# Kernel optimization log

Measured on AMD Instinct MI355X. Metric: run time of the kernel, lower is better.

Reference implementation:

```python
import jax, jax.numpy as jnp
import numpy as np

B, T, D = 4, 2048, 1024
H = 16
HD = D // H  # 64

def setup_inputs() -> dict:
    key = jax.random.key(0)
    k1, k2, k3, k4, k5 = jax.random.split(key, 5)
    s = 1.0 / np.sqrt(D)
    return {
        "x": jax.random.normal(k1, (B, T, D), dtype=jnp.float32),
        "Wqkv": jax.random.normal(k2, (D, 3 * D), dtype=jnp.float32) * s,
        "bqkv": jnp.zeros((3 * D,), dtype=jnp.float32),
        "Wproj": jax.random.normal(k3, (D, D), dtype=jnp.float32) * s,
        "bproj": jnp.zeros((D,), dtype=jnp.float32),
    }

def reference(x, Wqkv, bqkv, Wproj, bproj):
    Bq, Tq, C = x.shape
    qkv = x @ Wqkv + bqkv                       # [B,T,3D]
    qkv = qkv.reshape(Bq, Tq, 3, H, HD).transpose(2, 0, 3, 1, 4)  # [3,B,H,T,hd]
    q, k, v = qkv[0], qkv[1], qkv[2]
    scale = 1.0 / np.sqrt(HD)
    att = jnp.einsum("bhqd,bhkd->bhqk", q, k) * scale  # [B,H,T,T]
    causal = jnp.tril(jnp.ones((Tq, Tq), dtype=bool))
    att = jnp.where(causal[None, None], att, -jnp.inf)
    att = jax.nn.softmax(att, axis=-1)
    out = jnp.einsum("bhqk,bhkd->bhqd", att, v)        # [B,H,T,hd]
    out = out.transpose(0, 2, 1, 3).reshape(Bq, Tq, C)
    return out @ Wproj + bproj
```

## Files before the change

### kernel.cpp

```cpp
#include <hip/hip_runtime.h>

typedef float f32x4 __attribute__((ext_vector_type(4)));
typedef __bf16 bf16x8 __attribute__((ext_vector_type(8)));
typedef __bf16 bf16x4 __attribute__((ext_vector_type(4)));

#define B_ 4
#define T_ 2048
#define D_ 1024
#define H_ 16
#define HD_ 64

__device__ __forceinline__ void gload_lds16(const void* g, void* l) {
  __builtin_amdgcn_global_load_lds(
      (const __attribute__((address_space(1))) void*)g,
      (__attribute__((address_space(3))) void*)l, 16, 0, 0);
}

__global__ __launch_bounds__(256) void k_cvt_f32_bf16(
    const float* __restrict__ in, __bf16* __restrict__ out, int n4) {
  int i = blockIdx.x * blockDim.x + threadIdx.x;
  int stride = gridDim.x * blockDim.x;
  for (; i < n4; i += stride) {
    float4 v = reinterpret_cast<const float4*>(in)[i];
    bf16x4 o = { (__bf16)v.x, (__bf16)v.y, (__bf16)v.z, (__bf16)v.w };
    reinterpret_cast<bf16x4*>(out)[i] = o;
  }
}

template <typename Tin>
__global__ __launch_bounds__(256) void k_transpose_bf16(
    const Tin* __restrict__ in, __bf16* __restrict__ out,
    int R, int C, long inb, long outb) {
  __shared__ alignas(16) __bf16 lds[64 * 68];
  const int t = threadIdx.x;
  in  += (long)blockIdx.z * inb;
  out += (long)blockIdx.z * outb;
  const int r0 = blockIdx.y * 64, c0 = blockIdx.x * 64;
#pragma unroll
  for (int i = 0; i < 16; ++i) {
    int e = i * 256 + t, row = e >> 6, col = e & 63;
    lds[row * 68 + col] = (__bf16)(float)in[(long)(r0 + row) * C + c0 + col];
  }
  __syncthreads();
#pragma unroll
  for (int i = 0; i < 16; ++i) {
    int e = i * 256 + t, orow = e >> 6, ocol = e & 63;
    out[(long)(c0 + orow) * R + r0 + ocol] = lds[ocol * 68 + orow];
  }
}

template <int EPI>
__global__ __launch_bounds__(256) void k_gemm_bt(
    const __bf16* __restrict__ A, const __bf16* __restrict__ Bt,
    const float* __restrict__ bias, void* __restrict__ Cout,
    __bf16* __restrict__ vout, int M, int N, int K) {
  __shared__ alignas(16) __bf16 As[2][128 * 32];
  __shared__ alignas(16) __bf16 Bs[2][128 * 32];
  const int t = threadIdx.x;
  const int w = t >> 6, l = t & 63;
  const int g = l >> 4, r16 = l & 15;
  const int wr = w >> 1, wc = w & 1;
  const int m0 = blockIdx.y * 128, n0 = blockIdx.x * 128;

  f32x4 acc[4][4];
#pragma unroll
  for (int i = 0; i < 4; ++i)
#pragma unroll
    for (int j = 0; j < 4; ++j) acc[i][j] = (f32x4){0.f, 0.f, 0.f, 0.f};

  const int arow = t >> 2;
  const int acol = ((t & 3) ^ ((t >> 3) & 3)) * 8;
  const char* Ag = (const char*)(A + (long)(m0 + arow) * K + acol);
  const char* Bg = (const char*)(Bt + (long)(n0 + arow) * K + acol);
  const long rowskip = (long)64 * K * 2;
  const int rdsw = (g ^ ((r16 >> 1) & 3)) * 8;

  auto stage = [&](int buf, long koff) {
    char* AsW = (char*)As[buf] + w * 1024;
    char* BsW = (char*)Bs[buf] + w * 1024;
    gload_lds16(Ag + koff, AsW);
    gload_lds16(Ag + koff + rowskip, AsW + 4096);
    gload_lds16(Bg + koff, BsW);
    gload_lds16(Bg + koff + rowskip, BsW + 4096);
  };

  stage(0, 0);
  __syncthreads();

  for (int kt = 0; kt < K; kt += 32) {
    const int cur = (kt >> 5) & 1;
    if (kt + 32 < K) stage(cur ^ 1, (long)(kt + 32) * 2);
    bf16x8 af[4], bfr[4];
#pragma unroll
    for (int mi = 0; mi < 4; ++mi)
      af[mi] = *reinterpret_cast<const bf16x8*>(
          &As[cur][(wr * 64 + mi * 16 + r16) * 32 + rdsw]);
#pragma unroll
    for (int ni = 0; ni < 4; ++ni)
      bfr[ni] = *reinterpret_cast<const bf16x8*>(
          &Bs[cur][(wc * 64 + ni * 16 + r16) * 32 + rdsw]);
    __builtin_amdgcn_s_setprio(1);
#pragma unroll
    for (int mi = 0; mi < 4; ++mi)
#pragma unroll
      for (int ni = 0; ni < 4; ++ni)
        acc[mi][ni] = __builtin_amdgcn_mfma_f32_16x16x32_bf16(af[mi], bfr[ni], acc[mi][ni], 0, 0, 0);
    __builtin_amdgcn_s_setprio(0);
    __syncthreads();
  }

  if (EPI == 0) {
    const int which = n0 >> 10;
    __bf16* qkvb = (__bf16*)Cout;
#pragma unroll
    for (int mi = 0; mi < 4; ++mi) {
#pragma unroll
      for (int ni = 0; ni < 4; ++ni) {
        const int n = n0 + wc * 64 + ni * 16 + r16;
        const float bv = bias[n];
        f32x4 c = acc[mi][ni];
        const int rem = n & 1023, h = rem >> 6, hd = rem & 63;
        const int mbase = m0 + wr * 64 + mi * 16 + g * 4;
        const int b = mbase >> 11, tt0 = mbase & 2047;
        if (which < 2) {
#pragma unroll
          for (int r = 0; r < 4; ++r)
            qkvb[((long)((which * B_ + b) * H_ + h) * T_ + tt0 + r) * HD_ + hd] =
                (__bf16)(c[r] + bv);
        } else {
          bf16x4 pk = { (__bf16)(c[0] + bv), (__bf16)(c[1] + bv),
                        (__bf16)(c[2] + bv), (__bf16)(c[3] + bv) };
          *reinterpret_cast<bf16x4*>(
              &vout[(((long)b * H_ + h) * HD_ + hd) * T_ + tt0]) = pk;
        }
      }
    }
  } else {
    float* O = (float*)Cout;
#pragma unroll
    for (int mi = 0; mi < 4; ++mi) {
#pragma unroll
      for (int ni = 0; ni < 4; ++ni) {
        const int n = n0 + wc * 64 + ni * 16 + r16;
        const float bv = bias[n];
        f32x4 c = acc[mi][ni];
        const int mbase = m0 + wr * 64 + mi * 16 + g * 4;
#pragma unroll
        for (int r = 0; r < 4; ++r) O[(long)(mbase + r) * N + n] = c[r] + bv;
      }
    }
  }
}

__device__ __forceinline__ void soft_side(
    const f32x4 (&s)[4], float& lrun, char* pw, bool diag, int qrel,
    int g, int r16, bf16x8& pa0, bf16x8& pa1) {
  float p[4][4];
#pragma unroll
  for (int nf = 0; nf < 4; ++nf) {
#pragma unroll
    for (int rr = 0; rr < 4; ++rr) {
      float x = s[nf][rr];
      if (diag) x = (nf * 16 + 4 * g + rr <= qrel + r16) ? x : -1e30f;
      p[nf][rr] = exp2f(x);
    }
  }
  const float ps0 = (p[0][0] + p[0][1]) + (p[0][2] + p[0][3]);
  const float ps1 = (p[1][0] + p[1][1]) + (p[1][2] + p[1][3]);
  const float ps2 = (p[2][0] + p[2][1]) + (p[2][2] + p[2][3]);
  const float ps3 = (p[3][0] + p[3][1]) + (p[3][2] + p[3][3]);
  lrun += (ps0 + ps1) + (ps2 + ps3);

#pragma unroll
  for (int nf = 0; nf < 4; ++nf) {
    bf16x4 pk = { (__bf16)p[nf][0], (__bf16)p[nf][1],
                  (__bf16)p[nf][2], (__bf16)p[nf][3] };
    const int slot = 2 * nf + (g >> 1);
    *reinterpret_cast<bf16x4*>(
        pw + r16 * 128 + ((slot ^ (r16 & 7)) << 4) + (g & 1) * 8) = pk;
  }
  pa0 = *reinterpret_cast<const bf16x8*>(pw + r16 * 128 + ((g ^ (r16 & 7)) << 4));
  pa1 = *reinterpret_cast<const bf16x8*>(pw + r16 * 128 + (((4 + g) ^ (r16 & 7)) << 4));
}

__global__ __launch_bounds__(256) void k_attn(
    const __bf16* __restrict__ q, const __bf16* __restrict__ k,
    const __bf16* __restrict__ vt, __bf16* __restrict__ o) {
  __shared__ alignas(16) __bf16 Ks[2][64 * 64];
  __shared__ alignas(16) __bf16 Vs[2][64 * 64];
  __shared__ alignas(16) __bf16 Ps[4][16 * 64];
  const int t = threadIdx.x, w = t >> 6, l = t & 63;
  const int g = l >> 4, r16 = l & 15;
  const int bh = blockIdx.x, pr = blockIdx.y;
  const int qtA = 31 - pr, qtB = pr;
  const int qbaseA = qtA * 64 + w * 16;
  const int qbaseB = qtB * 64 + w * 16;
  const float sc = 0.125f * 1.44269504088896341f;

  auto scale8 = [&](bf16x8 v) {
    bf16x8 r;
#pragma unroll
    for (int j = 0; j < 8; ++j) r[j] = (__bf16)((float)v[j] * sc);
    return r;
  };
  const __bf16* qpA = q + ((long)bh * T_ + qbaseA + r16) * HD_ + g * 8;
  const bf16x8 aqA0 = scale8(*reinterpret_cast<const bf16x8*>(qpA));
  const bf16x8 aqA1 = scale8(*reinterpret_cast<const bf16x8*>(qpA + 32));
  const __bf16* qpB = q + ((long)bh * T_ + qbaseB + r16) * HD_ + g * 8;
  const bf16x8 aqB0 = scale8(*reinterpret_cast<const bf16x8*>(qpB));
  const bf16x8 aqB1 = scale8(*reinterpret_cast<const bf16x8*>(qpB + 32));

  f32x4 oA[4], oB[4];
  float lA = 0.f, lB = 0.f;
#pragma unroll
  for (int i = 0; i < 4; ++i) {
    oA[i] = (f32x4){0.f, 0.f, 0.f, 0.f};
    oB[i] = (f32x4){0.f, 0.f, 0.f, 0.f};
  }

  const int srow = t >> 3, sslot = t & 7;
  const int sswz = sslot ^ (srow & 7);
  const char* kg = (const char*)(k + ((long)bh * T_ + srow) * HD_) + sswz * 16;
  const char* vg = (const char*)(vt + ((long)bh * HD_ + srow) * T_) + sswz * 16;
  char* pw = (char*)&Ps[w][0];

  auto stage = [&](int buf, int kv0) {
    char* Kd = (char*)Ks[buf] + w * 1024;
    char* Vd = (char*)Vs[buf] + w * 1024;
    gload_lds16(kg + (long)kv0 * 128, Kd);
    gload_lds16(kg + (long)kv0 * 128 + 32 * 128, Kd + 4096);
    gload_lds16(vg + (long)kv0 * 2, Vd);
    gload_lds16(vg + (long)kv0 * 2 + 32 * (long)T_ * 2, Vd + 4096);
  };

  stage(0, 0);
  __syncthreads();

  const int ntile = qtA + 1;
  for (int it = 0; it < ntile; ++it) {
    const int cur = it & 1;
    if (it + 1 < ntile) stage(cur ^ 1, (it + 1) * 64);
    const char* Kc = (const char*)Ks[cur];
    const char* Vc = (const char*)Vs[cur];
    const bool doB = (it <= qtB);

    f32x4 sA[4], sB[4];
    __builtin_amdgcn_s_setprio(1);
#pragma unroll
    for (int nf = 0; nf < 4; ++nf) {
      const char* kb = Kc + (nf * 16 + r16) * 128;
      const bf16x8 b0 = *reinterpret_cast<const bf16x8*>(kb + ((g ^ (r16 & 7)) << 4));
      const bf16x8 b1 = *reinterpret_cast<const bf16x8*>(kb + (((4 + g) ^ (r16 & 7)) << 4));
      f32x4 z = (f32x4){0.f, 0.f, 0.f, 0.f};
      z = __builtin_amdgcn_mfma_f32_16x16x32_bf16(b0, aqA0, z, 0, 0, 0);
      z = __builtin_amdgcn_mfma_f32_16x16x32_bf16(b1, aqA1, z, 0, 0, 0);
      sA[nf] = z;
      if (doB) {
        f32x4 zb = (f32x4){0.f, 0.f, 0.f, 0.f};
        zb = __builtin_amdgcn_mfma_f32_16x16x32_bf16(b0, aqB0, zb, 0, 0, 0);
        zb = __builtin_amdgcn_mfma_f32_16x16x32_bf16(b1, aqB1, zb, 0, 0, 0);
        sB[nf] = zb;
      }
    }
    __builtin_amdgcn_s_setprio(0);

    bf16x8 paA0, paA1, paB0, paB1;
    soft_side(sA, lA, pw, it == qtA, qbaseA - it * 64, g, r16, paA0, paA1);
    if (doB)
      soft_side(sB, lB, pw, it == qtB, qbaseB - it * 64, g, r16, paB0, paB1);

    __builtin_amdgcn_s_setprio(1);
#pragma unroll
    for (int nf = 0; nf < 4; ++nf) {
      const char* vb = Vc + (nf * 16 + r16) * 128;
      const bf16x8 v0 = *reinterpret_cast<const bf16x8*>(vb + ((g ^ (r16 & 7)) << 4));
      const bf16x8 v1 = *reinterpret_cast<const bf16x8*>(vb + (((4 + g) ^ (r16 & 7)) << 4));
      oA[nf] = __builtin_amdgcn_mfma_f32_16x16x32_bf16(paA0, v0, oA[nf], 0, 0, 0);
      oA[nf] = __builtin_amdgcn_mfma_f32_16x16x32_bf16(paA1, v1, oA[nf], 0, 0, 0);
      if (doB) {
        oB[nf] = __builtin_amdgcn_mfma_f32_16x16x32_bf16(paB0, v0, oB[nf], 0, 0, 0);
        oB[nf] = __builtin_amdgcn_mfma_f32_16x16x32_bf16(paB1, v1, oB[nf], 0, 0, 0);
      }
    }
    __builtin_amdgcn_s_setprio(0);
    __syncthreads();
  }

  lA += __shfl_xor(lA, 16, 64);
  lA += __shfl_xor(lA, 32, 64);
  lB += __shfl_xor(lB, 16, 64);
  lB += __shfl_xor(lB, 32, 64);
  const float invA = 1.f / lA, invB = 1.f / lB;
  float invAq[4], invBq[4];
#pragma unroll
  for (int rr = 0; rr < 4; ++rr) {
    invAq[rr] = __shfl(invA, 4 * g + rr, 64);
    invBq[rr] = __shfl(invB, 4 * g + rr, 64);
  }
  const int b = bh >> 4, h = bh & 15;
#pragma unroll
  for (int nf = 0; nf < 4; ++nf) {
    const int hd = nf * 16 + r16;
#pragma unroll
    for (int rr = 0; rr < 4; ++rr) {
      const int ttA = qbaseA + g * 4 + rr;
      o[((long)b * T_ + ttA) * D_ + h * HD_ + hd] = (__bf16)(oA[nf][rr] * invAq[rr]);
      const int ttB = qbaseB + g * 4 + rr;
      o[((long)b * T_ + ttB) * D_ + h * HD_ + hd] = (__bf16)(oB[nf][rr] * invBq[rr]);
    }
  }
}

extern "C" void kernel_launch(void* const* d_in, const int* in_sizes, int n_in,
                              void* d_out, int out_size, void* d_ws, size_t ws_size,
                              hipStream_t stream) {
  (void)in_sizes; (void)n_in; (void)out_size; (void)ws_size;
  const float* x     = (const float*)d_in[0];
  const float* Wqkv  = (const float*)d_in[1];
  const float* bqkv  = (const float*)d_in[2];
  const float* Wproj = (const float*)d_in[3];
  const float* bproj = (const float*)d_in[4];
  float* out = (float*)d_out;

  const long MT = (long)B_ * T_;
  __bf16* xb     = (__bf16*)d_ws;
  __bf16* wqkvt  = xb + MT * D_;
  __bf16* wprojt = wqkvt + (long)3 * D_ * D_;
  __bf16* qkvb   = wprojt + (long)D_ * D_;
  __bf16* vtb    = qkvb + (long)2 * B_ * H_ * T_ * HD_;
  __bf16* attno  = vtb + (long)B_ * H_ * HD_ * T_;

  k_cvt_f32_bf16<<<2048, 256, 0, stream>>>(x, xb, (int)(MT * D_ / 4));
  k_transpose_bf16<float><<<dim3(48, 16, 1), 256, 0, stream>>>(Wqkv, wqkvt, D_, 3 * D_, 0, 0);
  k_transpose_bf16<float><<<dim3(16, 16, 1), 256, 0, stream>>>(Wproj, wprojt, D_, D_, 0, 0);
  k_gemm_bt<0><<<dim3(24, 64), 256, 0, stream>>>(xb, wqkvt, bqkv, qkvb, vtb, 8192, 3072, 1024);
  k_attn<<<dim3(64, 16), 256, 0, stream>>>(
      qkvb, qkvb + (long)B_ * H_ * T_ * HD_, vtb, attno);
  k_gemm_bt<1><<<dim3(8, 64), 256, 0, stream>>>(attno, wprojt, bproj, out, nullptr, 8192, 1024, 1024);
}
```

Measured before the change: 195.6 us.

## Redistribute softmax probabilities via lane permutes instead of LDS round-trip

Replaces the per-wave shared-memory write/read that transposed the P fragment into MFMA A-operand layout with packed bf16 conversions plus permlane32/permlane16 swaps done in registers. This removes the LDS scratch buffer and its store/load latency from the softmax-to-PV path. It also remaps blockIdx.y through a fixed permutation table to change the order in which the paired query tiles are scheduled. The register permutation must exactly reproduce the old layout or results will be wrong.

```diff
diff --git a/kernel.cpp b/kernel.cpp
--- a/kernel.cpp
+++ b/kernel.cpp
@@ -153,7 +153,7 @@
 }
 
 __device__ __forceinline__ void soft_side(
-    const f32x4 (&s)[4], float& lrun, char* pw, bool diag, int qrel,
+    const f32x4 (&s)[4], float& lrun, bool diag, int qrel,
     int g, int r16, bf16x8& pa0, bf16x8& pa1) {
   float p[4][4];
 #pragma unroll
@@ -171,16 +171,30 @@
   const float ps3 = (p[3][0] + p[3][1]) + (p[3][2] + p[3][3]);
   lrun += (ps0 + ps1) + (ps2 + ps3);
 
+  unsigned u[4][2];
 #pragma unroll
   for (int nf = 0; nf < 4; ++nf) {
-    bf16x4 pk = { (__bf16)p[nf][0], (__bf16)p[nf][1],
-                  (__bf16)p[nf][2], (__bf16)p[nf][3] };
-    const int slot = 2 * nf + (g >> 1);
-    *reinterpret_cast<bf16x4*>(
-        pw + r16 * 128 + ((slot ^ (r16 & 7)) << 4) + (g & 1) * 8) = pk;
-  }
-  pa0 = *reinterpret_cast<const bf16x8*>(pw + r16 * 128 + ((g ^ (r16 & 7)) << 4));
-  pa1 = *reinterpret_cast<const bf16x8*>(pw + r16 * 128 + (((4 + g) ^ (r16 & 7)) << 4));
+    asm("v_cvt_pk_bf16_f32 %0, %1, %2"
+        : "=v"(u[nf][0]) : "v"(p[nf][0]), "v"(p[nf][1]));
+    asm("v_cvt_pk_bf16_f32 %0, %1, %2"
+        : "=v"(u[nf][1]) : "v"(p[nf][2]), "v"(p[nf][3]));
+  }
+#pragma unroll
+  for (int j = 0; j < 2; ++j) {
+    asm("v_permlane32_swap_b32 %0, %1" : "+v"(u[0][j]), "+v"(u[1][j]));
+    asm("v_permlane32_swap_b32 %0, %1" : "+v"(u[2][j]), "+v"(u[3][j]));
+  }
+#pragma unroll
+  for (int j = 0; j < 2; ++j) {
+    asm("v_permlane16_swap_b32 %0, %1" : "+v"(u[0][j]), "+v"(u[1][j]));
+    asm("v_permlane16_swap_b32 %0, %1" : "+v"(u[2][j]), "+v"(u[3][j]));
+  }
+  union PU { unsigned w[4]; bf16x8 v; };
+  PU a0, a1;
+  a0.w[0] = u[0][0]; a0.w[1] = u[0][1]; a0.w[2] = u[1][0]; a0.w[3] = u[1][1];
+  a1.w[0] = u[2][0]; a1.w[1] = u[2][1]; a1.w[2] = u[3][0]; a1.w[3] = u[3][1];
+  pa0 = a0.v;
+  pa1 = a1.v;
 }
 
 __global__ __launch_bounds__(256) void k_attn(
@@ -188,10 +202,11 @@
     const __bf16* __restrict__ vt, __bf16* __restrict__ o) {
   __shared__ alignas(16) __bf16 Ks[2][64 * 64];
   __shared__ alignas(16) __bf16 Vs[2][64 * 64];
-  __shared__ alignas(16) __bf16 Ps[4][16 * 64];
   const int t = threadIdx.x, w = t >> 6, l = t & 63;
   const int g = l >> 4, r16 = l & 15;
-  const int bh = blockIdx.x, pr = blockIdx.y;
+  const int bh = blockIdx.x;
+  const int prmap[16] = {0, 2, 4, 6, 15, 13, 11, 9, 1, 3, 5, 7, 14, 12, 10, 8};
+  const int pr = prmap[blockIdx.y];
   const int qtA = 31 - pr, qtB = pr;
   const int qbaseA = qtA * 64 + w * 16;
   const int qbaseB = qtB * 64 + w * 16;
@@ -222,7 +237,6 @@
   const int sswz = sslot ^ (srow & 7);
   const char* kg = (const char*)(k + ((long)bh * T_ + srow) * HD_) + sswz * 16;
   const char* vg = (const char*)(vt + ((long)bh * HD_ + srow) * T_) + sswz * 16;
-  char* pw = (char*)&Ps[w][0];
 
   auto stage = [&](int buf, int kv0) {
     char* Kd = (char*)Ks[buf] + w * 1024;
@@ -265,9 +279,9 @@
     __builtin_amdgcn_s_setprio(0);
 
     bf16x8 paA0, paA1, paB0, paB1;
-    soft_side(sA, lA, pw, it == qtA, qbaseA - it * 64, g, r16, paA0, paA1);
+    soft_side(sA, lA, it == qtA, qbaseA - it * 64, g, r16, paA0, paA1);
     if (doB)
-      soft_side(sB, lB, pw, it == qtB, qbaseB - it * 64, g, r16, paB0, paB1);
+      soft_side(sB, lB, it == qtB, qbaseB - it * 64, g, r16, paB0, paB1);
 
     __builtin_amdgcn_s_setprio(1);
 #pragma unroll
```

After: 196.3 us. Within noise of the previous version (+0.3%).
